# Kernel tuning notes

Hardware: AMD Instinct MI355X
Metric: run time of the kernel (lower is better)

The kernel has to match this reference:

```python
import jax, jax.numpy as jnp
import numpy as np
import math
from jax import lax

B, M, T = 32, 80, 10000
EPS = 1e-6
DELTA_CLAMP = (0.001, 0.1)


def setup_inputs() -> dict:
    key = jax.random.key(0)
    k_mel, = jax.random.split(key, 1)
    # linear mel energies: non-negative
    mel = jax.random.uniform(k_mel, (B, M, T), dtype=jnp.float32)

    def full(v):
        return jnp.full((M,), v, dtype=jnp.float32)

    # exact init values from the torch module
    log_s = full(math.log(0.15 / (1 - 0.15)))
    log_alpha = full(math.log(0.99 / (1 - 0.99)))
    log_delta = full(math.log(0.01))
    log_r = full(math.log(0.1 / (1 - 0.1)))
    return {"mel": mel, "log_s": log_s, "log_alpha": log_alpha,
            "log_delta": log_delta, "log_r": log_r}


def reference(mel, log_s, log_alpha, log_delta, log_r):
    # per-channel coefficients, clamped exactly as in torch
    s = jnp.clip(jax.nn.sigmoid(log_s), 0.05, 0.3)            # (M,)
    alpha = jnp.clip(jax.nn.sigmoid(log_alpha), 0.9, 0.999)   # (M,)
    delta = jnp.clip(jnp.exp(log_delta), *DELTA_CLAMP)        # (M,)
    r = jnp.clip(jax.nn.sigmoid(log_r), 0.05, 0.25)           # (M,)

    # EMA smoother along time via scan. Torch inits smoother = mel[:,:,0]
    # and the t=0 update yields (1-s)*mel0 + s*mel0 = mel0, so we scan over
    # all T frames with init = mel[:,:,0].
    s_bm = s[None, :]                      # (1, M) broadcasts over (B, M)

    def step(smoother, x_t):
        new = (1.0 - s_bm) * smoother + s_bm * x_t
        return new, new

    xs = jnp.moveaxis(mel, -1, 0)          # (T, B, M)
    _, sm = lax.scan(step, mel[:, :, 0], xs)
    smoothed = jnp.moveaxis(sm, 0, -1)     # (B, M, T)

    alpha_c = alpha[None, :, None]
    delta_c = delta[None, :, None]
    r_c = r[None, :, None]

    gain = (EPS + smoothed) ** (-alpha_c)
    pcen = (mel * gain + delta_c) ** r_c - delta_c ** r_c
    return pcen
```

## Files before the change

kernel.cpp:

```cpp
#include <hip/hip_runtime.h>
#include <math.h>


constexpr int B_ = 32, M_ = 80, T_ = 10000;
constexpr int EPI   = 512;
constexpr int CHUNK = 1024;
constexpr int NCH   = (T_ + CHUNK - 1) / CHUNK;
constexpr float EPS_ = 1e-6f;

template <int CTRL, int ROWMASK, bool BC>
__device__ __forceinline__ float fdpp(float oldv, float v) {
    return __int_as_float(__builtin_amdgcn_update_dpp(
        __float_as_int(oldv), __float_as_int(v), CTRL, ROWMASK, 0xF, BC));
}
__device__ __forceinline__ float rdlane(float v, int l) {
    return __int_as_float(__builtin_amdgcn_readlane(__float_as_int(v), l));
}

__global__ __launch_bounds__(256) void pcen_kernel(
    const float* __restrict__ mel,
    const float* __restrict__ log_s,
    const float* __restrict__ log_alpha,
    const float* __restrict__ log_delta,
    const float* __restrict__ log_r,
    float* __restrict__ out)
{
    const int lane = threadIdx.x & 63;
    const int wv   = threadIdx.x >> 6;
    const int gw   = blockIdx.x * 4 + wv;
    if (gw >= B_ * M_ * NCH) return;
    const int row = gw / NCH;
    const int c   = gw - row * NCH;
    const int m   = row % M_;

    const float* mp = mel + (size_t)row * T_;
    float*       op = out + (size_t)row * T_;
    const int start = c * CHUNK;

    const int base0 = start + lane * 8;
    const int base1 = base0 + EPI;
    const bool act0 = base0 < T_;
    const bool act1 = base1 < T_;
    float4 xa0 = make_float4(0,0,0,0), xb0 = xa0, xa1 = xa0, xb1 = xa0;
    if (act0) { xa0 = *(const float4*)(mp + base0);
                xb0 = *(const float4*)(mp + base0 + 4); }
    if (act1) { xa1 = *(const float4*)(mp + base1);
                xb1 = *(const float4*)(mp + base1 + 4); }
    float xh = 0.f;
    if (c > 0) xh = mp[start - 64 + lane];

    float s = 1.f / (1.f + __expf(-log_s[m]));         s = fminf(fmaxf(s, 0.05f), 0.3f);
    float alpha = 1.f / (1.f + __expf(-log_alpha[m])); alpha = fminf(fmaxf(alpha, 0.9f), 0.999f);
    float delta = __expf(log_delta[m]);                delta = fminf(fmaxf(delta, 0.001f), 0.1f);
    float r = 1.f / (1.f + __expf(-log_r[m]));         r = fminf(fmaxf(r, 0.05f), 0.25f);
    const float dr = __expf(r * __logf(delta));

    const float a  = 1.f - s;
    const float la = __logf(a);
    const float a2 = a*a, a3 = a2*a, a4 = a2*a2,
                a5 = a4*a, a6 = a4*a2, a7 = a4*a3, a8 = a4*a4;
    const float a16 = a8*a8, a32 = a16*a16;
    const float inv_a8 = 1.f / a8;
    const int   j16 = lane & 15;
    const float qlane  = __expf(la * (float)(8 * (j16 + 1)));
    const float a8lane = __expf(la * (float)(8 * lane));

    auto pcen1 = [&](float x, float y) {
        float g = __expf(-alpha * __logf(y + EPS_));
        float z = fmaf(x, g, delta);
        return __expf(r * __logf(z)) - dr;
    };

    auto iter = [&](const float4& xa, const float4& xb, int bas, bool act,
                    float ypv) -> float {
        float l0 = s * xa.x;
        float l1 = fmaf(a, l0, s * xa.y);
        float l2 = fmaf(a, l1, s * xa.z);
        float l3 = fmaf(a, l2, s * xa.w);
        float l4 = fmaf(a, l3, s * xb.x);
        float l5 = fmaf(a, l4, s * xb.y);
        float l6 = fmaf(a, l5, s * xb.z);
        float l7 = fmaf(a, l6, s * xb.w);

        float W = l7, t;
        t = fdpp<0x111, 0xF, true>(0.f, W);  W = fmaf(a8,  t, W);
        t = fdpp<0x112, 0xF, true>(0.f, W);  W = fmaf(a16, t, W);
        t = fdpp<0x114, 0xF, true>(0.f, W);  W = fmaf(a32, t, W);
        float Bv = fdpp<0x142, 0xE, false>(0.f, W);
        W = fmaf(qlane, Bv, W);

        float E = (W - l7) * inv_a8;
        float C = fmaf(a8lane, ypv, E);
        float ynext = rdlane(W, 63);

        if (act) {
            float4 o1, o2;
            o1.x = pcen1(xa.x, fmaf(a,  C, l0));
            o1.y = pcen1(xa.y, fmaf(a2, C, l1));
            o1.z = pcen1(xa.z, fmaf(a3, C, l2));
            o1.w = pcen1(xa.w, fmaf(a4, C, l3));
            o2.x = pcen1(xb.x, fmaf(a5, C, l4));
            o2.y = pcen1(xb.y, fmaf(a6, C, l5));
            o2.z = pcen1(xb.z, fmaf(a7, C, l6));
            o2.w = pcen1(xb.w, fmaf(a8, C, l7));
            *(float4*)(op + bas)     = o1;
            *(float4*)(op + bas + 4) = o2;
        }
        return ynext;
    };

    float yprev;
    if (c == 0) {
        yprev = rdlane(xa0.x, 0);
    } else {
        float u = s * xh * __expf(la * (float)(63 - lane));
        u += __shfl_xor(u, 32);
        u += __shfl_xor(u, 16);
        u += __shfl_xor(u, 8);
        u += __shfl_xor(u, 4);
        u += __shfl_xor(u, 2);
        u += __shfl_xor(u, 1);
        yprev = u;
    }

    yprev = iter(xa0, xb0, base0, act0, yprev);
    (void)  iter(xa1, xb1, base1, act1, yprev);
}

extern "C" void kernel_launch(void* const* d_in, const int* in_sizes, int n_in,
                              void* d_out, int out_size, void* d_ws, size_t ws_size,
                              hipStream_t stream) {
    const float* mel       = (const float*)d_in[0];
    const float* log_s     = (const float*)d_in[1];
    const float* log_alpha = (const float*)d_in[2];
    const float* log_delta = (const float*)d_in[3];
    const float* log_r     = (const float*)d_in[4];
    float* out = (float*)d_out;

    const int nwaves = B_ * M_ * NCH;
    dim3 grid((nwaves + 3) / 4);
    pcen_kernel<<<grid, 256, 0, stream>>>(mel, log_s, log_alpha, log_delta,
                                          log_r, out);
}
```

Before: 187.6 us.

## Process five chunks per wave with prefetch, native exp2/log2, nontemporal stores

Each wave now covers half a row (five chunks of 1024 frames) rather than a single chunk. The EMA carry is passed between chunks in registers, and the loads for the next chunk are issued while the current one is being computed. This removes the per-chunk head reconstruction and cuts the wave count from 25600 to 5120, which lowers occupancy and parallelism. The kernel also switches to native exp2/log2 intrinsics and writes its output with nontemporal stores.

```diff
diff --git a/kernel.cpp b/kernel.cpp
--- a/kernel.cpp
+++ b/kernel.cpp
@@ -5,8 +5,10 @@
 constexpr int B_ = 32, M_ = 80, T_ = 10000;
 constexpr int EPI   = 512;
 constexpr int CHUNK = 1024;
-constexpr int NCH   = (T_ + CHUNK - 1) / CHUNK;
+constexpr int HALF  = 5;
 constexpr float EPS_ = 1e-6f;
+
+typedef float f32x4 __attribute__((ext_vector_type(4)));
 
 template <int CTRL, int ROWMASK, bool BC>
 __device__ __forceinline__ float fdpp(float oldv, float v) {
@@ -16,6 +18,8 @@
 __device__ __forceinline__ float rdlane(float v, int l) {
     return __int_as_float(__builtin_amdgcn_readlane(__float_as_int(v), l));
 }
+__device__ __forceinline__ float fexp2(float x) { return __builtin_amdgcn_exp2f(x); }
+__device__ __forceinline__ float flog2(float x) { return __builtin_amdgcn_logf(x); }
 
 __global__ __launch_bounds__(256) void pcen_kernel(
     const float* __restrict__ mel,
@@ -28,50 +32,47 @@
     const int lane = threadIdx.x & 63;
     const int wv   = threadIdx.x >> 6;
     const int gw   = blockIdx.x * 4 + wv;
-    if (gw >= B_ * M_ * NCH) return;
-    const int row = gw / NCH;
-    const int c   = gw - row * NCH;
-    const int m   = row % M_;
+    if (gw >= B_ * M_ * 2) return;
+    const int row  = gw >> 1;
+    const int half = gw & 1;
+    const int m    = row % M_;
 
     const float* mp = mel + (size_t)row * T_;
     float*       op = out + (size_t)row * T_;
-    const int start = c * CHUNK;
+    const int start = half * (HALF * CHUNK);
 
-    const int base0 = start + lane * 8;
-    const int base1 = base0 + EPI;
-    const bool act0 = base0 < T_;
-    const bool act1 = base1 < T_;
-    float4 xa0 = make_float4(0,0,0,0), xb0 = xa0, xa1 = xa0, xb1 = xa0;
-    if (act0) { xa0 = *(const float4*)(mp + base0);
-                xb0 = *(const float4*)(mp + base0 + 4); }
-    if (act1) { xa1 = *(const float4*)(mp + base1);
-                xb1 = *(const float4*)(mp + base1 + 4); }
+    int b0 = start + lane * 8;
+    f32x4 ca = *(const f32x4*)(mp + b0);
+    f32x4 cb = *(const f32x4*)(mp + b0 + 4);
+    f32x4 cc = *(const f32x4*)(mp + b0 + EPI);
+    f32x4 cd = *(const f32x4*)(mp + b0 + EPI + 4);
     float xh = 0.f;
-    if (c > 0) xh = mp[start - 64 + lane];
+    if (half) xh = mp[start - 64 + lane];
 
     float s = 1.f / (1.f + __expf(-log_s[m]));         s = fminf(fmaxf(s, 0.05f), 0.3f);
     float alpha = 1.f / (1.f + __expf(-log_alpha[m])); alpha = fminf(fmaxf(alpha, 0.9f), 0.999f);
     float delta = __expf(log_delta[m]);                delta = fminf(fmaxf(delta, 0.001f), 0.1f);
     float r = 1.f / (1.f + __expf(-log_r[m]));         r = fminf(fmaxf(r, 0.05f), 0.25f);
-    const float dr = __expf(r * __logf(delta));
+    const float dr  = fexp2(r * flog2(delta));
+    const float nal = -alpha;
 
-    const float a  = 1.f - s;
-    const float la = __logf(a);
+    const float a   = 1.f - s;
+    const float la2 = flog2(a);
     const float a2 = a*a, a3 = a2*a, a4 = a2*a2,
                 a5 = a4*a, a6 = a4*a2, a7 = a4*a3, a8 = a4*a4;
     const float a16 = a8*a8, a32 = a16*a16;
     const float inv_a8 = 1.f / a8;
     const int   j16 = lane & 15;
-    const float qlane  = __expf(la * (float)(8 * (j16 + 1)));
-    const float a8lane = __expf(la * (float)(8 * lane));
+    const float qlane  = fexp2(la2 * (float)(8 * (j16 + 1)));
+    const float a8lane = fexp2(la2 * (float)(8 * lane));
 
     auto pcen1 = [&](float x, float y) {
-        float g = __expf(-alpha * __logf(y + EPS_));
+        float g = fexp2(nal * flog2(y + EPS_));
         float z = fmaf(x, g, delta);
-        return __expf(r * __logf(z)) - dr;
+        return fexp2(r * flog2(z)) - dr;
     };
 
-    auto iter = [&](const float4& xa, const float4& xb, int bas, bool act,
+    auto iter = [&](const f32x4& xa, const f32x4& xb, int bas, bool act,
                     float ypv) -> float {
         float l0 = s * xa.x;
         float l1 = fmaf(a, l0, s * xa.y);
@@ -94,7 +95,7 @@
         float ynext = rdlane(W, 63);
 
         if (act) {
-            float4 o1, o2;
+            f32x4 o1, o2;
             o1.x = pcen1(xa.x, fmaf(a,  C, l0));
             o1.y = pcen1(xa.y, fmaf(a2, C, l1));
             o1.z = pcen1(xa.z, fmaf(a3, C, l2));
@@ -103,17 +104,17 @@
             o2.y = pcen1(xb.y, fmaf(a6, C, l5));
             o2.z = pcen1(xb.z, fmaf(a7, C, l6));
             o2.w = pcen1(xb.w, fmaf(a8, C, l7));
-            *(float4*)(op + bas)     = o1;
-            *(float4*)(op + bas + 4) = o2;
+            __builtin_nontemporal_store(o1, (f32x4*)(op + bas));
+            __builtin_nontemporal_store(o2, (f32x4*)(op + bas + 4));
         }
         return ynext;
     };
 
     float yprev;
-    if (c == 0) {
-        yprev = rdlane(xa0.x, 0);
+    if (half == 0) {
+        yprev = rdlane(ca.x, 0);
     } else {
-        float u = s * xh * __expf(la * (float)(63 - lane));
+        float u = s * xh * fexp2(la2 * (float)(63 - lane));
         u += __shfl_xor(u, 32);
         u += __shfl_xor(u, 16);
         u += __shfl_xor(u, 8);
@@ -123,8 +124,25 @@
         yprev = u;
     }
 
-    yprev = iter(xa0, xb0, base0, act0, yprev);
-    (void)  iter(xa1, xb1, base1, act1, yprev);
+    #pragma unroll
+    for (int k = 0; k < HALF; ++k) {
+        f32x4 na = {0.f,0.f,0.f,0.f}, nb = na, nc = na, nd = na;
+        if (k + 1 < HALF) {
+            const int pb = b0 + CHUNK;
+            const bool p0 = pb < T_;
+            const bool p1 = pb + EPI < T_;
+            if (p0) { na = *(const f32x4*)(mp + pb);
+                      nb = *(const f32x4*)(mp + pb + 4); }
+            if (p1) { nc = *(const f32x4*)(mp + pb + EPI);
+                      nd = *(const f32x4*)(mp + pb + EPI + 4); }
+        }
+        const bool act0 = b0 < T_;
+        const bool act1 = b0 + EPI < T_;
+        yprev = iter(ca, cb, b0, act0, yprev);
+        yprev = iter(cc, cd, b0 + EPI, act1, yprev);
+        ca = na; cb = nb; cc = nc; cd = nd;
+        b0 += CHUNK;
+    }
 }
 
 extern "C" void kernel_launch(void* const* d_in, const int* in_sizes, int n_in,
@@ -137,7 +155,7 @@
     const float* log_r     = (const float*)d_in[4];
     float* out = (float*)d_out;
 
-    const int nwaves = B_ * M_ * NCH;
+    const int nwaves = B_ * M_ * 2;
     dim3 grid((nwaves + 3) / 4);
     pcen_kernel<<<grid, 256, 0, stream>>>(mel, log_s, log_alpha, log_delta,
                                           log_r, out);
```

New measurement: 208.0 us. 1.11x slower.
